# Optimization experiments

Hardware: AMD Instinct MI355X
Metric: run time of the kernel (lower is better)

Reference implementation:

```python
import jax, jax.numpy as jnp
import numpy as np

D_MODEL = 1024
D_STATE = 16
D_CONV = 4
EXPAND = 2
D_INNER = EXPAND * D_MODEL  # 2048
B_SZ = 4
SEQ_L = 2048


def setup_inputs() -> dict:
    key = jax.random.key(0)
    ks = jax.random.split(key, 8)
    x = jax.random.normal(ks[0], (B_SZ, SEQ_L, D_MODEL), dtype=jnp.float32)
    # nn.Linear(d_model, 2*d_inner, bias=False): weight [2*d_inner, d_model]
    W_in = jax.random.normal(ks[1], (2 * D_INNER, D_MODEL), dtype=jnp.float32) * (1.0 / np.sqrt(D_MODEL))
    # depthwise Conv1d weight [d_inner, 1, d_conv] -> stored as [d_inner, d_conv]
    conv_w = jax.random.normal(ks[2], (D_INNER, D_CONV), dtype=jnp.float32) * (1.0 / np.sqrt(D_CONV))
    conv_b = jax.random.normal(ks[3], (D_INNER,), dtype=jnp.float32) * 0.01
    W_out = jax.random.normal(ks[4], (D_MODEL, D_INNER), dtype=jnp.float32) * (1.0 / np.sqrt(D_INNER))
    A = jnp.eye(D_STATE, dtype=jnp.float32)
    Bmat = jax.random.normal(ks[5], (D_STATE, D_INNER), dtype=jnp.float32) * 0.01
    Cmat = jax.random.normal(ks[6], (D_STATE, D_INNER), dtype=jnp.float32) * 0.01
    return {"x": x, "W_in": W_in, "conv_w": conv_w, "conv_b": conv_b,
            "W_out": W_out, "A": A, "Bmat": Bmat, "Cmat": Cmat}


def _causal_depthwise_conv(x_bld, conv_w, conv_b):
    # x_bld: [B, L, C]; conv_w: [C, k]; matches torch Conv1d(groups=C, padding=k-1) sliced to [:L]
    C, k = conv_w.shape
    lhs = jnp.transpose(x_bld, (0, 2, 1))            # [B, C, L]
    rhs = conv_w[:, None, :]                          # [C, 1, k]
    out = jax.lax.conv_general_dilated(
        lhs, rhs, window_strides=(1,), padding=[(k - 1, 0)],
        feature_group_count=C,
        dimension_numbers=("NCH", "OIH", "NCH"))
    out = out + conv_b[None, :, None]
    return jnp.transpose(out, (0, 2, 1))              # [B, L, C]


def reference(x, W_in, conv_w, conv_b, W_out, A, Bmat, Cmat):
    B, L, _ = x.shape
    d_state = A.shape[0]
    xz = x @ W_in.T                                   # [B, L, 2*d_inner]
    x_part, z = jnp.split(xz, 2, axis=-1)             # each [B, L, d_inner]
    x_conv = jax.nn.silu(_causal_depthwise_conv(x_part, conv_w, conv_b))
    # precompute input drive u_t = x_t @ B.T for all t
    u = jnp.einsum("bld,sd->bls", x_part, Bmat)       # [B, L, d_state]

    def step(s, u_t):                                 # s: [B, d_state]
        s = s @ A.T + u_t
        return s, s

    s0 = jnp.zeros((B, d_state), dtype=x.dtype)
    _, states = jax.lax.scan(step, s0, jnp.transpose(u, (1, 0, 2)))  # [L, B, d_state]
    states = jnp.transpose(states, (1, 0, 2))         # [B, L, d_state]
    state_proj = jnp.einsum("bls,sd->bld", states, Cmat)  # [B, L, d_inner]
    y = (x_conv + state_proj) * jax.nn.sigmoid(z)     # [B, L, d_inner]
    return y @ W_out.T                                # [B, L, d_model]
```

## Files before the change

kernel.cpp:

```cpp
#include <hip/hip_runtime.h>

#define D_MODEL 1024
#define D_STATE 16
#define D_CONV  4
#define D_INNER 2048
#define B_SZ    4
#define SEQ_L   2048
#define ROWS    (B_SZ * SEQ_L)
#define N_XZ    (2 * D_INNER)

typedef unsigned short u16;
typedef unsigned int   u32;
typedef float f32x4 __attribute__((ext_vector_type(4)));
typedef short s16x8 __attribute__((ext_vector_type(8)));
typedef u16   u16x8 __attribute__((ext_vector_type(8)));
typedef u16   u16x4 __attribute__((ext_vector_type(4)));

__device__ __forceinline__ u16 f2bf(float f) {
  union { float f; u32 u; } v; v.f = f;
  u32 r = v.u + 0x7fffu + ((v.u >> 16) & 1u);
  return (u16)(r >> 16);
}
__device__ __forceinline__ float bf2f(u16 h) {
  union { u32 u; float f; } v; v.u = ((u32)h) << 16; return v.f;
}
__device__ __forceinline__ float sigmoidf_(float x) {
  return 1.0f / (1.0f + __expf(-x));
}

__global__ __launch_bounds__(256) void k_f2bf4(
    const float* __restrict__ a, u16* __restrict__ ao, int na4,
    const float* __restrict__ b, u16* __restrict__ bo, int nb4,
    const float* __restrict__ c, u16* __restrict__ co, int nc4,
    const float* __restrict__ e, u16* __restrict__ eo, int ne4)
{
  int i = blockIdx.x * 256 + threadIdx.x;
  const float* s; u16* d; int j;
  if (i < na4)                              { s = a; d = ao; j = i; }
  else if (i - na4 < nb4)                   { s = b; d = bo; j = i - na4; }
  else if (i - na4 - nb4 < nc4)             { s = c; d = co; j = i - na4 - nb4; }
  else if (i - na4 - nb4 - nc4 < ne4)       { s = e; d = eo; j = i - na4 - nb4 - nc4; }
  else return;
  f32x4 v = ((const f32x4*)s)[j];
  u16x4 o;
  o[0] = f2bf(v[0]); o[1] = f2bf(v[1]); o[2] = f2bf(v[2]); o[3] = f2bf(v[3]);
  ((u16x4*)d)[j] = o;
}

__global__ __launch_bounds__(512, 2) void k_g201(
    const u16* __restrict__ A,
    const u16* __restrict__ B,
    u16* __restrict__ C,
    int M, int N, int K, int nbx)
{
  __shared__ __align__(16) u16 lA[2][256 * 64];
  __shared__ __align__(16) u16 lB[2][256 * 64];

  const int t    = threadIdx.x;
  const int lane = t & 63;
  const int wave = t >> 6;
  const int wr   = wave >> 2;
  const int wc   = wave & 3;
  const int lrow = lane & 15;
  const int lch  = lane >> 4;

  const int xcd = blockIdx.x & 7;
  const int sub = blockIdx.x >> 3;
  const int msz = (M >> 8) >> 2;
  const int nsz = nbx >> 1;
  const int sm  = sub / nsz;
  const int sn  = sub - sm * nsz;
  const int bm  = ((xcd >> 1) * msz + sm) * 256;
  const int bn  = ((xcd & 1) * nsz + sn) * 256;
  const int NT  = K / 64;

  const int rl0 = t >> 3;
  const int cc  = t & 7;
  int rowG[4][2];
  rowG[0][0] = rl0;        rowG[0][1] = rl0 + 128;
  rowG[1][0] = rl0 + 64;   rowG[1][1] = rl0 + 192;
  rowG[2][0] = rl0;        rowG[2][1] = rl0 + 64;
  rowG[3][0] = rl0 + 128;  rowG[3][1] = rl0 + 192;
  const u16* srcG[4][2];
  u32 dstG[4][2];
#pragma unroll
  for (int g = 0; g < 4; ++g)
#pragma unroll
    for (int i = 0; i < 2; ++i) {
      int row = rowG[g][i];
      const u16* base = (g < 2) ? A + (size_t)(bm + row) * K
                                : B + (size_t)(bn + row) * K;
      srcG[g][i] = base + ((cc ^ (row & 7)) << 3);
      dstG[g][i] = (u32)(row * 64 + cc * 8);
    }

  auto stage = [&](int g, int buf, int kt) {
    u16* dst0 = (g < 2) ? &lA[buf][dstG[g][0]] : &lB[buf][dstG[g][0]];
    u16* dst1 = (g < 2) ? &lA[buf][dstG[g][1]] : &lB[buf][dstG[g][1]];
    __builtin_amdgcn_global_load_lds(
        (const __attribute__((address_space(1))) void*)(srcG[g][0] + kt * 64),
        (__attribute__((address_space(3))) void*)dst0, 16, 0, 0);
    __builtin_amdgcn_global_load_lds(
        (const __attribute__((address_space(1))) void*)(srcG[g][1] + kt * 64),
        (__attribute__((address_space(3))) void*)dst1, 16, 0, 0);
  };

  u32 aoff[8], boff[4], ck[2];
#pragma unroll
  for (int mi = 0; mi < 8; ++mi)
    aoff[mi] = (u32)((wr * 128 + mi * 16 + lrow) * 128);
#pragma unroll
  for (int ni = 0; ni < 4; ++ni)
    boff[ni] = (u32)((wc * 64 + ni * 16 + lrow) * 128);
#pragma unroll
  for (int ks = 0; ks < 2; ++ks)
    ck[ks] = (u32)((((ks * 4 + lch) ^ (lrow & 7)) << 4));
  const u32 baseA = (u32)(size_t)(__attribute__((address_space(3))) void*)&lA[0][0];
  const u32 baseB = (u32)(size_t)(__attribute__((address_space(3))) void*)&lB[0][0];

  f32x4 acc[8][4] = {};
  s16x8 av[4], bv0[4], bv1[4];

  stage(0, 0, 0); stage(1, 0, 0); stage(2, 0, 0); stage(3, 0, 0);
  stage(0, 1, 1); stage(2, 1, 1);
  asm volatile("s_waitcnt vmcnt(4)" ::: "memory");
  __builtin_amdgcn_s_barrier();

  for (int tt = 0; tt < NT; ++tt) {
    const int cur = tt & 1, nxt = cur ^ 1;
    const u32 bA = baseA + (u32)cur * 32768u;
    const u32 bB = baseB + (u32)cur * 32768u;
    const bool s1 = (tt + 1 < NT), s2 = (tt + 2 < NT);

#pragma unroll
    for (int mi = 0; mi < 4; ++mi) {
      u32 ad = bA + aoff[mi] + ck[0];
      asm volatile("ds_read_b128 %0, %1" : "=v"(av[mi]) : "v"(ad));
    }
#pragma unroll
    for (int ni = 0; ni < 4; ++ni) {
      u32 ad = bB + boff[ni] + ck[0];
      asm volatile("ds_read_b128 %0, %1" : "=v"(bv0[ni]) : "v"(ad));
    }
    if (s1) stage(3, nxt, tt + 1);
    __builtin_amdgcn_s_barrier();
    asm volatile("s_waitcnt lgkmcnt(0)" ::: "memory");
    __builtin_amdgcn_sched_barrier(0);
    __builtin_amdgcn_s_setprio(1);
#pragma unroll
    for (int mi = 0; mi < 4; ++mi)
#pragma unroll
      for (int ni = 0; ni < 4; ++ni)
        acc[mi][ni] = __builtin_amdgcn_mfma_f32_16x16x32_bf16(av[mi], bv0[ni], acc[mi][ni], 0, 0, 0);
    __builtin_amdgcn_s_setprio(0);
    __builtin_amdgcn_s_barrier();

#pragma unroll
    for (int mi = 0; mi < 4; ++mi) {
      u32 ad = bA + aoff[mi] + ck[1];
      asm volatile("ds_read_b128 %0, %1" : "=v"(av[mi]) : "v"(ad));
    }
#pragma unroll
    for (int ni = 0; ni < 4; ++ni) {
      u32 ad = bB + boff[ni] + ck[1];
      asm volatile("ds_read_b128 %0, %1" : "=v"(bv1[ni]) : "v"(ad));
    }
    if (s1) stage(1, nxt, tt + 1);
    __builtin_amdgcn_s_barrier();
    asm volatile("s_waitcnt lgkmcnt(0)" ::: "memory");
    __builtin_amdgcn_sched_barrier(0);
    __builtin_amdgcn_s_setprio(1);
#pragma unroll
    for (int mi = 0; mi < 4; ++mi)
#pragma unroll
      for (int ni = 0; ni < 4; ++ni)
        acc[mi][ni] = __builtin_amdgcn_mfma_f32_16x16x32_bf16(av[mi], bv1[ni], acc[mi][ni], 0, 0, 0);
    __builtin_amdgcn_s_setprio(0);
    asm volatile("s_waitcnt vmcnt(6)" ::: "memory");
    __builtin_amdgcn_s_barrier();

#pragma unroll
    for (int mi = 0; mi < 4; ++mi) {
      u32 ad = bA + aoff[4 + mi] + ck[0];
      asm volatile("ds_read_b128 %0, %1" : "=v"(av[mi]) : "v"(ad));
    }
    if (s2) stage(0, cur, tt + 2);
    __builtin_amdgcn_s_barrier();
    asm volatile("s_waitcnt lgkmcnt(0)" ::: "memory");
    __builtin_amdgcn_sched_barrier(0);
    __builtin_amdgcn_s_setprio(1);
#pragma unroll
    for (int mi = 0; mi < 4; ++mi)
#pragma unroll
      for (int ni = 0; ni < 4; ++ni)
        acc[4 + mi][ni] = __builtin_amdgcn_mfma_f32_16x16x32_bf16(av[mi], bv0[ni], acc[4 + mi][ni], 0, 0, 0);
    __builtin_amdgcn_s_setprio(0);
    __builtin_amdgcn_s_barrier();

#pragma unroll
    for (int mi = 0; mi < 4; ++mi) {
      u32 ad = bA + aoff[4 + mi] + ck[1];
      asm volatile("ds_read_b128 %0, %1" : "=v"(av[mi]) : "v"(ad));
    }
    if (s2) stage(2, cur, tt + 2);
    __builtin_amdgcn_s_barrier();
    asm volatile("s_waitcnt lgkmcnt(0)" ::: "memory");
    __builtin_amdgcn_sched_barrier(0);
    __builtin_amdgcn_s_setprio(1);
#pragma unroll
    for (int mi = 0; mi < 4; ++mi)
#pragma unroll
      for (int ni = 0; ni < 4; ++ni)
        acc[4 + mi][ni] = __builtin_amdgcn_mfma_f32_16x16x32_bf16(av[mi], bv1[ni], acc[4 + mi][ni], 0, 0, 0);
    __builtin_amdgcn_s_setprio(0);
    if (s2)      asm volatile("s_waitcnt vmcnt(6)" ::: "memory");
    else if (s1) asm volatile("s_waitcnt vmcnt(0)" ::: "memory");
    __builtin_amdgcn_s_barrier();
  }

  const int crow0 = (lane >> 4) * 4;
#pragma unroll
  for (int mi = 0; mi < 8; ++mi)
#pragma unroll
    for (int ni = 0; ni < 4; ++ni)
#pragma unroll
      for (int r = 0; r < 4; ++r) {
        int row = bm + wr * 128 + mi * 16 + crow0 + r;
        int col = bn + wc * 64 + ni * 16 + lrow;
        C[(size_t)row * N + col] = f2bf(acc[mi][ni][r]);
      }
}

template<bool OUT_BF16>
__global__ __launch_bounds__(256, 2) void k_gemm_f(
    const u16* __restrict__ A, const u16* __restrict__ B,
    void* __restrict__ Cv, int M, int N, int K, int nbx)
{
  __shared__ __align__(16) u16 lA[3][128 * 32];
  __shared__ __align__(16) u16 lB[3][256 * 32];

  const int t    = threadIdx.x;
  const int lane = t & 63;
  const int wave = t >> 6;
  const int wr   = wave >> 1;
  const int wc   = wave & 1;
  const int lrow = lane & 15;
  const int lch  = lane >> 4;

  const int xcd = blockIdx.x & 7;
  const int sub = blockIdx.x >> 3;
  const int msz = (M >> 7) >> 2;
  const int nsz = nbx >> 1;
  const int sm  = sub / nsz;
  const int sn  = sub - sm * nsz;
  const int bm  = ((xcd >> 1) * msz + sm) * 128;
  const int bn  = ((xcd & 1) * nsz + sn) * 256;
  const int NT  = K / 32;

  const int ca0 = t, ca1 = t + 256;
  const u16* srcA0 = A + (size_t)(bm + (ca0 >> 2)) * K + ((ca0 & 3) ^ ((ca0 >> 3) & 3)) * 8;
  const u16* srcA1 = A + (size_t)(bm + (ca1 >> 2)) * K + ((ca1 & 3) ^ ((ca1 >> 3) & 3)) * 8;
  const u16* srcB[4];
#pragma unroll
  for (int i = 0; i < 4; ++i) {
    int c = t + i * 256;
    srcB[i] = B + (size_t)(bn + (c >> 2)) * K + ((c & 3) ^ ((c >> 3) & 3)) * 8;
  }

  auto stageA = [&](int sl, int kt) {
    __builtin_amdgcn_global_load_lds(
        (const __attribute__((address_space(1))) void*)(srcA0 + kt * 32),
        (__attribute__((address_space(3))) void*)&lA[sl][ca0 * 8], 16, 0, 0);
    __builtin_amdgcn_global_load_lds(
        (const __attribute__((address_space(1))) void*)(srcA1 + kt * 32),
        (__attribute__((address_space(3))) void*)&lA[sl][ca1 * 8], 16, 0, 0);
  };
  auto stageB = [&](int sl, int kt) {
#pragma unroll
    for (int i = 0; i < 4; ++i) {
      int c = t + i * 256;
      __builtin_amdgcn_global_load_lds(
          (const __attribute__((address_space(1))) void*)(srcB[i] + kt * 32),
          (__attribute__((address_space(3))) void*)&lB[sl][c * 8], 16, 0, 0);
    }
  };

  u32 offA[4], offB[8];
#pragma unroll
  for (int m = 0; m < 4; ++m) {
    int ra = wr * 64 + m * 16 + lrow;
    offA[m] = (u32)(ra * 64 + ((lch ^ ((ra >> 1) & 3)) << 4));
  }
#pragma unroll
  for (int n = 0; n < 8; ++n) {
    int rb = wc * 128 + n * 16 + lrow;
    offB[n] = (u32)(rb * 64 + ((lch ^ ((rb >> 1) & 3)) << 4));
  }
  const u32 baseA = (u32)(size_t)(__attribute__((address_space(3))) void*)&lA[0][0];
  const u32 baseB = (u32)(size_t)(__attribute__((address_space(3))) void*)&lB[0][0];

  f32x4 acc[4][8] = {};
  s16x8 av[4], bv[8];

  stageA(0, 0); stageB(0, 0);
  stageA(1, 1); stageB(1, 1);
  asm volatile("s_waitcnt vmcnt(6)" ::: "memory");
  __builtin_amdgcn_s_barrier();

  int slot = 0;
  for (int tt = 0; tt < NT; ++tt) {
    const int nslot = (slot == 0) ? 2 : slot - 1;
    const u32 bA = baseA + (u32)slot * 8192u;
    const u32 bB = baseB + (u32)slot * 16384u;
    const bool st = (tt + 2 < NT);
#pragma unroll
    for (int m = 0; m < 4; ++m) {
      u32 ad = bA + offA[m];
      asm volatile("ds_read_b128 %0, %1" : "=v"(av[m]) : "v"(ad));
    }
#pragma unroll
    for (int n = 0; n < 4; ++n) {
      u32 ad = bB + offB[n];
      asm volatile("ds_read_b128 %0, %1" : "=v"(bv[n]) : "v"(ad));
    }
    if (st) stageA(nslot, tt + 2);
    __builtin_amdgcn_s_barrier();
    asm volatile("s_waitcnt lgkmcnt(0)" ::: "memory");
    __builtin_amdgcn_sched_barrier(0);
    __builtin_amdgcn_s_setprio(1);
#pragma unroll
    for (int m = 0; m < 4; ++m)
#pragma unroll
      for (int n = 0; n < 4; ++n)
        acc[m][n] = __builtin_amdgcn_mfma_f32_16x16x32_bf16(av[m], bv[n], acc[m][n], 0, 0, 0);
    __builtin_amdgcn_s_setprio(0);
    __builtin_amdgcn_s_barrier();
#pragma unroll
    for (int n = 4; n < 8; ++n) {
      u32 ad = bB + offB[n];
      asm volatile("ds_read_b128 %0, %1" : "=v"(bv[n]) : "v"(ad));
    }
    if (st) stageB(nslot, tt + 2);
    __builtin_amdgcn_s_barrier();
    asm volatile("s_waitcnt lgkmcnt(0)" ::: "memory");
    __builtin_amdgcn_sched_barrier(0);
    __builtin_amdgcn_s_setprio(1);
#pragma unroll
    for (int m = 0; m < 4; ++m)
#pragma unroll
      for (int n = 4; n < 8; ++n)
        acc[m][n] = __builtin_amdgcn_mfma_f32_16x16x32_bf16(av[m], bv[n], acc[m][n], 0, 0, 0);
    __builtin_amdgcn_s_setprio(0);
    if (st)                asm volatile("s_waitcnt vmcnt(6)" ::: "memory");
    else if (tt + 1 < NT)  asm volatile("s_waitcnt vmcnt(0)" ::: "memory");
    __builtin_amdgcn_s_barrier();
    slot = (slot == 2) ? 0 : slot + 1;
  }

  const int crow0 = (lane >> 4) * 4;
  if constexpr (OUT_BF16) {
    u16* C = (u16*)Cv;
#pragma unroll
    for (int m = 0; m < 4; ++m)
#pragma unroll
      for (int n = 0; n < 8; ++n)
#pragma unroll
        for (int r = 0; r < 4; ++r) {
          int row = bm + wr * 64 + m * 16 + crow0 + r;
          int col = bn + wc * 128 + n * 16 + lrow;
          C[(size_t)row * N + col] = f2bf(acc[m][n][r]);
        }
  } else {
    float* C = (float*)Cv;
#pragma unroll
    for (int m = 0; m < 4; ++m)
#pragma unroll
      for (int n = 0; n < 8; ++n)
#pragma unroll
        for (int r = 0; r < 4; ++r) {
          int row = bm + wr * 64 + m * 16 + crow0 + r;
          int col = bn + wc * 128 + n * 16 + lrow;
          C[(size_t)row * N + col] = acc[m][n][r];
        }
  }
}

__global__ __launch_bounds__(256) void k_u_mfma(
    const u16* __restrict__ xz, const u16* __restrict__ Bbf,
    float* __restrict__ u)
{
  const int lane = threadIdx.x & 63;
  const int wave = threadIdx.x >> 6;
  const int row0 = blockIdx.x * 64 + wave * 16;
  const int ar   = lane & 15;
  const int ak   = (lane >> 4) * 8;
  const u16* xp = xz + (size_t)(row0 + ar) * N_XZ + ak;
  const u16* bp = Bbf + (size_t)ar * D_INNER + ak;
  f32x4 acc = {};
#pragma unroll 8
  for (int k = 0; k < D_INNER; k += 32) {
    s16x8 av = *(const s16x8*)(xp + k);
    s16x8 bv = *(const s16x8*)(bp + k);
    acc = __builtin_amdgcn_mfma_f32_16x16x32_bf16(av, bv, acc, 0, 0, 0);
  }
#pragma unroll
  for (int r = 0; r < 4; ++r)
    u[(size_t)(row0 + (lane >> 4) * 4 + r) * D_STATE + ar] = acc[r];
}

__global__ __launch_bounds__(64) void k_scan(
    const float* __restrict__ u, float* __restrict__ states)
{
  const int blk  = blockIdx.x;
  const int b    = blk >> 4;
  const int s    = blk & 15;
  const int lane = threadIdx.x;
  const float* up = u + (size_t)b * SEQ_L * D_STATE + s;
  float* sp = states + (size_t)b * SEQ_L * D_STATE + s;
  const int t0 = lane * (SEQ_L / 64);
  float v[32];
  float run = 0.0f;
#pragma unroll
  for (int i = 0; i < 32; ++i) { run += up[(size_t)(t0 + i) * D_STATE]; v[i] = run; }
  float tot = run;
  float pre = tot;
#pragma unroll
  for (int off = 1; off < 64; off <<= 1) {
    float n = __shfl_up(pre, off);
    if (lane >= off) pre += n;
  }
  pre -= tot;
#pragma unroll
  for (int i = 0; i < 32; ++i) sp[(size_t)(t0 + i) * D_STATE] = v[i] + pre;
}

__global__ __launch_bounds__(256) void k_fused_y(
    const u16* __restrict__ xz, const float* __restrict__ conv_w,
    const float* __restrict__ conv_b, const float* __restrict__ states,
    const float* __restrict__ Cmat, u16* __restrict__ y)
{
  const int t    = threadIdx.x;
  const int row0 = blockIdx.x * 4;
  const int l0   = row0 & (SEQ_L - 1);
  const int d0   = t * 8;

  float xin[7][8];
#pragma unroll
  for (int r = 0; r < 7; ++r) {
    int l = l0 + r - 3;
    if (l >= 0) {
      u16x8 v = *(const u16x8*)(xz + (size_t)(row0 + r - 3) * N_XZ + d0);
#pragma unroll
      for (int j = 0; j < 8; ++j) xin[r][j] = bf2f(v[j]);
    } else {
#pragma unroll
      for (int j = 0; j < 8; ++j) xin[r][j] = 0.0f;
    }
  }

  float cw[8][4];
#pragma unroll
  for (int j = 0; j < 8; ++j) {
    f32x4 w = ((const f32x4*)conv_w)[d0 + j];
#pragma unroll
    for (int k = 0; k < 4; ++k) cw[j][k] = w[k];
  }
  f32x4 cb0 = *(const f32x4*)(conv_b + d0);
  f32x4 cb1 = *(const f32x4*)(conv_b + d0 + 4);

  float xc[4][8];
#pragma unroll
  for (int rr = 0; rr < 4; ++rr)
#pragma unroll
    for (int j = 0; j < 8; ++j) {
      float v = (j < 4) ? cb0[j] : cb1[j - 4];
#pragma unroll
      for (int k = 0; k < 4; ++k) v += xin[rr + k][j] * cw[j][k];
      xc[rr][j] = v * sigmoidf_(v);
    }

  float st[4][16];
#pragma unroll
  for (int rr = 0; rr < 4; ++rr) {
    const f32x4* s4 = (const f32x4*)(states + (size_t)(row0 + rr) * D_STATE);
#pragma unroll
    for (int q = 0; q < 4; ++q) {
      f32x4 v = s4[q];
      st[rr][q * 4 + 0] = v[0]; st[rr][q * 4 + 1] = v[1];
      st[rr][q * 4 + 2] = v[2]; st[rr][q * 4 + 3] = v[3];
    }
  }
  float sp[4][8] = {};
#pragma unroll
  for (int s = 0; s < 16; ++s) {
    const float* cp = Cmat + (size_t)s * D_INNER + d0;
    f32x4 c0 = *(const f32x4*)cp;
    f32x4 c1 = *(const f32x4*)(cp + 4);
#pragma unroll
    for (int rr = 0; rr < 4; ++rr)
#pragma unroll
      for (int j = 0; j < 4; ++j) {
        sp[rr][j]     += st[rr][s] * c0[j];
        sp[rr][4 + j] += st[rr][s] * c1[j];
      }
  }
#pragma unroll
  for (int rr = 0; rr < 4; ++rr) {
    u16x8 zv = *(const u16x8*)(xz + (size_t)(row0 + rr) * N_XZ + D_INNER + d0);
    u16x8 o;
#pragma unroll
    for (int j = 0; j < 8; ++j)
      o[j] = f2bf((xc[rr][j] + sp[rr][j]) * sigmoidf_(bf2f(zv[j])));
    *(u16x8*)(y + (size_t)(row0 + rr) * D_INNER + d0) = o;
  }
}

extern "C" void kernel_launch(void* const* d_in, const int* in_sizes, int n_in,
                              void* d_out, int out_size, void* d_ws, size_t ws_size,
                              hipStream_t stream) {
  const float* x      = (const float*)d_in[0];
  const float* W_in   = (const float*)d_in[1];
  const float* conv_w = (const float*)d_in[2];
  const float* conv_b = (const float*)d_in[3];
  const float* W_out  = (const float*)d_in[4];
  const float* Bmat   = (const float*)d_in[6];
  const float* Cmat   = (const float*)d_in[7];
  float* out = (float*)d_out;

  char* ws = (char*)d_ws;
  u16*   xzbf   = (u16*)  (ws + 0);
  u16*   ybf    = (u16*)  (ws + 67108864);
  u16*   xbf    = (u16*)  (ws + 100663296);
  u16*   wibf   = (u16*)  (ws + 117440512);
  u16*   wobf   = (u16*)  (ws + 125829120);
  float* u      = (float*)(ws + 130023424);
  float* states = (float*)(ws + 130547712);
  u16*   bmbf   = (u16*)  (ws + 131072000);

  {
    int na4 = ROWS * D_MODEL / 4, nb4 = N_XZ * D_MODEL / 4,
        nc4 = D_MODEL * D_INNER / 4, ne4 = D_STATE * D_INNER / 4;
    int tot = na4 + nb4 + nc4 + ne4;
    k_f2bf4<<<(tot + 255) / 256, 256, 0, stream>>>(
        x, xbf, na4, W_in, wibf, nb4, W_out, wobf, nc4, Bmat, bmbf, ne4);
  }

  k_g201<<<512, 512, 0, stream>>>(xbf, wibf, xzbf, ROWS, N_XZ, D_MODEL, N_XZ / 256);

  k_u_mfma<<<ROWS / 64, 256, 0, stream>>>(xzbf, bmbf, u);
  k_scan<<<B_SZ * D_STATE, 64, 0, stream>>>(u, states);

  k_fused_y<<<ROWS / 4, 256, 0, stream>>>(xzbf, conv_w, conv_b, states, Cmat, ybf);

  k_gemm_f<false><<<256, 256, 0, stream>>>(ybf, wobf, out, ROWS, D_MODEL, D_INNER, D_MODEL / 256);
}
```

Baseline: 191.8 us.

## Fuse x fp32-to-bf16 conversion into input GEMM A-tile staging

```diff
diff --git a/kernel.cpp b/kernel.cpp
--- a/kernel.cpp
+++ b/kernel.cpp
@@ -28,18 +28,16 @@
   return 1.0f / (1.0f + __expf(-x));
 }
 
-__global__ __launch_bounds__(256) void k_f2bf4(
+__global__ __launch_bounds__(256) void k_f2bf3(
     const float* __restrict__ a, u16* __restrict__ ao, int na4,
     const float* __restrict__ b, u16* __restrict__ bo, int nb4,
-    const float* __restrict__ c, u16* __restrict__ co, int nc4,
-    const float* __restrict__ e, u16* __restrict__ eo, int ne4)
+    const float* __restrict__ c, u16* __restrict__ co, int nc4)
 {
   int i = blockIdx.x * 256 + threadIdx.x;
   const float* s; u16* d; int j;
-  if (i < na4)                              { s = a; d = ao; j = i; }
-  else if (i - na4 < nb4)                   { s = b; d = bo; j = i - na4; }
-  else if (i - na4 - nb4 < nc4)             { s = c; d = co; j = i - na4 - nb4; }
-  else if (i - na4 - nb4 - nc4 < ne4)       { s = e; d = eo; j = i - na4 - nb4 - nc4; }
+  if (i < na4)                        { s = a; d = ao; j = i; }
+  else if (i - na4 < nb4)             { s = b; d = bo; j = i - na4; }
+  else if (i - na4 - nb4 < nc4)       { s = c; d = co; j = i - na4 - nb4; }
   else return;
   f32x4 v = ((const f32x4*)s)[j];
   u16x4 o;
@@ -48,7 +46,7 @@
 }
 
 __global__ __launch_bounds__(512, 2) void k_g201(
-    const u16* __restrict__ A,
+    const float* __restrict__ X,
     const u16* __restrict__ B,
     u16* __restrict__ C,
     int M, int N, int K, int nbx)
@@ -74,35 +72,55 @@
   const int bn  = ((xcd & 1) * nsz + sn) * 256;
   const int NT  = K / 64;
 
+  const float* srcA[4];
+  u32 dstA[4];
+#pragma unroll
+  for (int i = 0; i < 4; ++i) {
+    int c    = t + i * 512;
+    int row  = c >> 3;
+    int col8 = c & 7;
+    srcA[i] = X + (size_t)(bm + row) * K + col8 * 8;
+    dstA[i] = (u32)(row * 64 + ((col8 ^ (row & 7)) << 3));
+  }
   const int rl0 = t >> 3;
   const int cc  = t & 7;
-  int rowG[4][2];
-  rowG[0][0] = rl0;        rowG[0][1] = rl0 + 128;
-  rowG[1][0] = rl0 + 64;   rowG[1][1] = rl0 + 192;
-  rowG[2][0] = rl0;        rowG[2][1] = rl0 + 64;
-  rowG[3][0] = rl0 + 128;  rowG[3][1] = rl0 + 192;
-  const u16* srcG[4][2];
-  u32 dstG[4][2];
-#pragma unroll
-  for (int g = 0; g < 4; ++g)
-#pragma unroll
-    for (int i = 0; i < 2; ++i) {
-      int row = rowG[g][i];
-      const u16* base = (g < 2) ? A + (size_t)(bm + row) * K
-                                : B + (size_t)(bn + row) * K;
-      srcG[g][i] = base + ((cc ^ (row & 7)) << 3);
-      dstG[g][i] = (u32)(row * 64 + cc * 8);
-    }
-
-  auto stage = [&](int g, int buf, int kt) {
-    u16* dst0 = (g < 2) ? &lA[buf][dstG[g][0]] : &lB[buf][dstG[g][0]];
-    u16* dst1 = (g < 2) ? &lA[buf][dstG[g][1]] : &lB[buf][dstG[g][1]];
-    __builtin_amdgcn_global_load_lds(
-        (const __attribute__((address_space(1))) void*)(srcG[g][0] + kt * 64),
-        (__attribute__((address_space(3))) void*)dst0, 16, 0, 0);
-    __builtin_amdgcn_global_load_lds(
-        (const __attribute__((address_space(1))) void*)(srcG[g][1] + kt * 64),
-        (__attribute__((address_space(3))) void*)dst1, 16, 0, 0);
+  int rowB[4] = { rl0, rl0 + 64, rl0 + 128, rl0 + 192 };
+  const u16* srcB[4];
+  u32 dstB[4];
+#pragma unroll
+  for (int i = 0; i < 4; ++i) {
+    int row = rowB[i];
+    srcB[i] = B + (size_t)(bn + row) * K + ((cc ^ (row & 7)) << 3);
+    dstB[i] = (u32)(row * 64 + cc * 8);
+  }
+  auto stageB = [&](int buf, int kt) {
+#pragma unroll
+    for (int i = 0; i < 4; ++i)
+      __builtin_amdgcn_global_load_lds(
+          (const __attribute__((address_space(1))) void*)(srcB[i] + kt * 64),
+          (__attribute__((address_space(3))) void*)&lB[buf][dstB[i]], 16, 0, 0);
+  };
+
+  f32x4 ald[4][2];
+  auto loadA = [&](int kt) {
+#pragma unroll
+    for (int i = 0; i < 4; ++i) {
+      const float* p = srcA[i] + kt * 64;
+      ald[i][0] = *(const f32x4*)p;
+      ald[i][1] = *(const f32x4*)(p + 4);
+    }
+  };
+  auto writeA = [&](int buf) {
+#pragma unroll
+    for (int i = 0; i < 4; ++i) {
+      u16x8 w;
+#pragma unroll
+      for (int j = 0; j < 4; ++j) {
+        w[j]     = f2bf(ald[i][0][j]);
+        w[4 + j] = f2bf(ald[i][1][j]);
+      }
+      *(u16x8*)&lA[buf][dstA[i]] = w;
+    }
   };
 
   u32 aoff[8], boff[4], ck[2];
@@ -121,28 +139,44 @@
   f32x4 acc[8][4] = {};
   s16x8 av[4], bv0[4], bv1[4];
 
-  stage(0, 0, 0); stage(1, 0, 0); stage(2, 0, 0); stage(3, 0, 0);
-  stage(0, 1, 1); stage(2, 1, 1);
-  asm volatile("s_waitcnt vmcnt(4)" ::: "memory");
+  loadA(0);
+  stageB(0, 0);
+  f32x4 sav[4][2];
+  {
+#pragma unroll
+    for (int i = 0; i < 4; ++i) {
+      const float* p = srcA[i] + 64;
+      sav[i][0] = *(const f32x4*)p;
+      sav[i][1] = *(const f32x4*)(p + 4);
+    }
+  }
+  stageB(1, 1);
+  asm volatile("s_waitcnt vmcnt(16)" ::: "memory");
+  writeA(0);
+#pragma unroll
+  for (int i = 0; i < 4; ++i) { ald[i][0] = sav[i][0]; ald[i][1] = sav[i][1]; }
+  asm volatile("s_waitcnt vmcnt(8)" ::: "memory");
+  asm volatile("s_waitcnt lgkmcnt(0)" ::: "memory");
+  __builtin_amdgcn_sched_barrier(0);
   __builtin_amdgcn_s_barrier();
 
   for (int tt = 0; tt < NT; ++tt) {
     const int cur = tt & 1, nxt = cur ^ 1;
     const u32 bA = baseA + (u32)cur * 32768u;
     const u32 bB = baseB + (u32)cur * 32768u;
-    const bool s1 = (tt + 1 < NT), s2 = (tt + 2 < NT);
-
+    const bool s1 = (tt + 1 < NT);
+
+#pragma unroll
+    for (int ni = 0; ni < 4; ++ni) {
+      u32 ad = bB + boff[ni] + ck[0];
+      asm volatile("ds_read_b128 %0, %1" : "=v"(bv0[ni]) : "v"(ad));
+    }
 #pragma unroll
     for (int mi = 0; mi < 4; ++mi) {
       u32 ad = bA + aoff[mi] + ck[0];
       asm volatile("ds_read_b128 %0, %1" : "=v"(av[mi]) : "v"(ad));
     }
-#pragma unroll
-    for (int ni = 0; ni < 4; ++ni) {
-      u32 ad = bB + boff[ni] + ck[0];
-      asm volatile("ds_read_b128 %0, %1" : "=v"(bv0[ni]) : "v"(ad));
-    }
-    if (s1) stage(3, nxt, tt + 1);
+    if (s1 && tt > 0) loadA(tt + 1);
     __builtin_amdgcn_s_barrier();
     asm volatile("s_waitcnt lgkmcnt(0)" ::: "memory");
     __builtin_amdgcn_sched_barrier(0);
@@ -156,16 +190,16 @@
     __builtin_amdgcn_s_barrier();
 
 #pragma unroll
+    for (int ni = 0; ni < 4; ++ni) {
+      u32 ad = bB + boff[ni] + ck[1];
+      asm volatile("ds_read_b128 %0, %1" : "=v"(bv1[ni]) : "v"(ad));
+    }
+#pragma unroll
     for (int mi = 0; mi < 4; ++mi) {
       u32 ad = bA + aoff[mi] + ck[1];
       asm volatile("ds_read_b128 %0, %1" : "=v"(av[mi]) : "v"(ad));
     }
-#pragma unroll
-    for (int ni = 0; ni < 4; ++ni) {
-      u32 ad = bB + boff[ni] + ck[1];
-      asm volatile("ds_read_b128 %0, %1" : "=v"(bv1[ni]) : "v"(ad));
-    }
-    if (s1) stage(1, nxt, tt + 1);
+    if (s1 && tt > 0) stageB(nxt, tt + 1);
     __builtin_amdgcn_s_barrier();
     asm volatile("s_waitcnt lgkmcnt(0)" ::: "memory");
     __builtin_amdgcn_sched_barrier(0);
@@ -176,7 +210,6 @@
       for (int ni = 0; ni < 4; ++ni)
         acc[mi][ni] = __builtin_amdgcn_mfma_f32_16x16x32_bf16(av[mi], bv1[ni], acc[mi][ni], 0, 0, 0);
     __builtin_amdgcn_s_setprio(0);
-    asm volatile("s_waitcnt vmcnt(6)" ::: "memory");
     __builtin_amdgcn_s_barrier();
 
 #pragma unroll
@@ -184,7 +217,6 @@
       u32 ad = bA + aoff[4 + mi] + ck[0];
       asm volatile("ds_read_b128 %0, %1" : "=v"(av[mi]) : "v"(ad));
     }
-    if (s2) stage(0, cur, tt + 2);
     __builtin_amdgcn_s_barrier();
     asm volatile("s_waitcnt lgkmcnt(0)" ::: "memory");
     __builtin_amdgcn_sched_barrier(0);
@@ -202,7 +234,11 @@
       u32 ad = bA + aoff[4 + mi] + ck[1];
       asm volatile("ds_read_b128 %0, %1" : "=v"(av[mi]) : "v"(ad));
     }
-    if (s2) stage(2, cur, tt + 2);
+    if (s1) {
+      if (tt > 0) { asm volatile("s_waitcnt vmcnt(4)" ::: "memory"); }
+      else        { asm volatile("s_waitcnt vmcnt(0)" ::: "memory"); }
+      writeA(nxt);
+    }
     __builtin_amdgcn_s_barrier();
     asm volatile("s_waitcnt lgkmcnt(0)" ::: "memory");
     __builtin_amdgcn_sched_barrier(0);
@@ -213,8 +249,7 @@
       for (int ni = 0; ni < 4; ++ni)
         acc[4 + mi][ni] = __builtin_amdgcn_mfma_f32_16x16x32_bf16(av[mi], bv1[ni], acc[4 + mi][ni], 0, 0, 0);
     __builtin_amdgcn_s_setprio(0);
-    if (s2)      asm volatile("s_waitcnt vmcnt(6)" ::: "memory");
-    else if (s1) asm volatile("s_waitcnt vmcnt(0)" ::: "memory");
+    if (s1) asm volatile("s_waitcnt vmcnt(0)" ::: "memory");
     __builtin_amdgcn_s_barrier();
   }
 
@@ -314,14 +349,14 @@
     const u32 bB = baseB + (u32)slot * 16384u;
     const bool st = (tt + 2 < NT);
 #pragma unroll
+    for (int n = 0; n < 4; ++n) {
+      u32 ad = bB + offB[n];
+      asm volatile("ds_read_b128 %0, %1" : "=v"(bv[n]) : "v"(ad));
+    }
+#pragma unroll
     for (int m = 0; m < 4; ++m) {
       u32 ad = bA + offA[m];
       asm volatile("ds_read_b128 %0, %1" : "=v"(av[m]) : "v"(ad));
-    }
-#pragma unroll
-    for (int n = 0; n < 4; ++n) {
-      u32 ad = bB + offB[n];
-      asm volatile("ds_read_b128 %0, %1" : "=v"(bv[n]) : "v"(ad));
     }
     if (st) stageA(nslot, tt + 2);
     __builtin_amdgcn_s_barrier();
@@ -439,24 +474,8 @@
     const float* __restrict__ conv_b, const float* __restrict__ states,
     const float* __restrict__ Cmat, u16* __restrict__ y)
 {
-  const int t    = threadIdx.x;
-  const int row0 = blockIdx.x * 4;
-  const int l0   = row0 & (SEQ_L - 1);
-  const int d0   = t * 8;
-
-  float xin[7][8];
-#pragma unroll
-  for (int r = 0; r < 7; ++r) {
-    int l = l0 + r - 3;
-    if (l >= 0) {
-      u16x8 v = *(const u16x8*)(xz + (size_t)(row0 + r - 3) * N_XZ + d0);
-#pragma unroll
-      for (int j = 0; j < 8; ++j) xin[r][j] = bf2f(v[j]);
-    } else {
-#pragma unroll
-      for (int j = 0; j < 8; ++j) xin[r][j] = 0.0f;
-    }
-  }
+  const int t  = threadIdx.x;
+  const int d0 = t * 8;
 
   float cw[8][4];
 #pragma unroll
@@ -468,50 +487,69 @@
   f32x4 cb0 = *(const f32x4*)(conv_b + d0);
   f32x4 cb1 = *(const f32x4*)(conv_b + d0 + 4);
 
-  float xc[4][8];
-#pragma unroll
-  for (int rr = 0; rr < 4; ++rr)
-#pragma unroll
-    for (int j = 0; j < 8; ++j) {
-      float v = (j < 4) ? cb0[j] : cb1[j - 4];
-#pragma unroll
-      for (int k = 0; k < 4; ++k) v += xin[rr + k][j] * cw[j][k];
-      xc[rr][j] = v * sigmoidf_(v);
-    }
-
-  float st[4][16];
-#pragma unroll
-  for (int rr = 0; rr < 4; ++rr) {
-    const f32x4* s4 = (const f32x4*)(states + (size_t)(row0 + rr) * D_STATE);
-#pragma unroll
-    for (int q = 0; q < 4; ++q) {
-      f32x4 v = s4[q];
-      st[rr][q * 4 + 0] = v[0]; st[rr][q * 4 + 1] = v[1];
-      st[rr][q * 4 + 2] = v[2]; st[rr][q * 4 + 3] = v[3];
-    }
-  }
-  float sp[4][8] = {};
-#pragma unroll
-  for (int s = 0; s < 16; ++s) {
-    const float* cp = Cmat + (size_t)s * D_INNER + d0;
-    f32x4 c0 = *(const f32x4*)cp;
-    f32x4 c1 = *(const f32x4*)(cp + 4);
+  for (int ch = 0; ch < 4; ++ch) {
+    const int row0 = blockIdx.x * 16 + ch * 4;
+    const int l0   = row0 & (SEQ_L - 1);
+
+    float xin[7][8];
+#pragma unroll
+    for (int r = 0; r < 7; ++r) {
+      int l = l0 + r - 3;
+      if (l >= 0) {
+        u16x8 v = *(const u16x8*)(xz + (size_t)(row0 + r - 3) * N_XZ + d0);
+#pragma unroll
+        for (int j = 0; j < 8; ++j) xin[r][j] = bf2f(v[j]);
+      } else {
+#pragma unroll
+        for (int j = 0; j < 8; ++j) xin[r][j] = 0.0f;
+      }
+    }
+
+    float xc[4][8];
 #pragma unroll
     for (int rr = 0; rr < 4; ++rr)
 #pragma unroll
-      for (int j = 0; j < 4; ++j) {
-        sp[rr][j]     += st[rr][s] * c0[j];
-        sp[rr][4 + j] += st[rr][s] * c1[j];
+      for (int j = 0; j < 8; ++j) {
+        float v = (j < 4) ? cb0[j] : cb1[j - 4];
+#pragma unroll
+        for (int k = 0; k < 4; ++k) v += xin[rr + k][j] * cw[j][k];
+        xc[rr][j] = v * sigmoidf_(v);
       }
-  }
-#pragma unroll
-  for (int rr = 0; rr < 4; ++rr) {
-    u16x8 zv = *(const u16x8*)(xz + (size_t)(row0 + rr) * N_XZ + D_INNER + d0);
-    u16x8 o;
-#pragma unroll
-    for (int j = 0; j < 8; ++j)
-      o[j] = f2bf((xc[rr][j] + sp[rr][j]) * sigmoidf_(bf2f(zv[j])));
-    *(u16x8*)(y + (size_t)(row0 + rr) * D_INNER + d0) = o;
+
+    float st[4][16];
+#pragma unroll
+    for (int rr = 0; rr < 4; ++rr) {
+      const f32x4* s4 = (const f32x4*)(states + (size_t)(row0 + rr) * D_STATE);
+#pragma unroll
+      for (int q = 0; q < 4; ++q) {
+        f32x4 v = s4[q];
+        st[rr][q * 4 + 0] = v[0]; st[rr][q * 4 + 1] = v[1];
+        st[rr][q * 4 + 2] = v[2]; st[rr][q * 4 + 3] = v[3];
+      }
+    }
+    float sp[4][8] = {};
+#pragma unroll
+    for (int s = 0; s < 16; ++s) {
+      const float* cp = Cmat + (size_t)s * D_INNER + d0;
+      f32x4 c0 = *(const f32x4*)cp;
+      f32x4 c1 = *(const f32x4*)(cp + 4);
+#pragma unroll
+      for (int rr = 0; rr < 4; ++rr)
+#pragma unroll
+        for (int j = 0; j < 4; ++j) {
+          sp[rr][j]     += st[rr][s] * c0[j];
+          sp[rr][4 + j] += st[rr][s] * c1[j];
+        }
+    }
+#pragma unroll
+    for (int rr = 0; rr < 4; ++rr) {
+      u16x8 zv = *(const u16x8*)(xz + (size_t)(row0 + rr) * N_XZ + D_INNER + d0);
+      u16x8 o;
+#pragma unroll
+      for (int j = 0; j < 8; ++j)
+        o[j] = f2bf((xc[rr][j] + sp[rr][j]) * sigmoidf_(bf2f(zv[j])));
+      *(u16x8*)(y + (size_t)(row0 + rr) * D_INNER + d0) = o;
+    }
   }
 }
 
@@ -530,7 +568,6 @@
   char* ws = (char*)d_ws;
   u16*   xzbf   = (u16*)  (ws + 0);
   u16*   ybf    = (u16*)  (ws + 67108864);
-  u16*   xbf    = (u16*)  (ws + 100663296);
   u16*   wibf   = (u16*)  (ws + 117440512);
   u16*   wobf   = (u16*)  (ws + 125829120);
   float* u      = (float*)(ws + 130023424);
@@ -538,19 +575,19 @@
   u16*   bmbf   = (u16*)  (ws + 131072000);
 
   {
-    int na4 = ROWS * D_MODEL / 4, nb4 = N_XZ * D_MODEL / 4,
-        nc4 = D_MODEL * D_INNER / 4, ne4 = D_STATE * D_INNER / 4;
-    int tot = na4 + nb4 + nc4 + ne4;
-    k_f2bf4<<<(tot + 255) / 256, 256, 0, stream>>>(
-        x, xbf, na4, W_in, wibf, nb4, W_out, wobf, nc4, Bmat, bmbf, ne4);
-  }
-
-  k_g201<<<512, 512, 0, stream>>>(xbf, wibf, xzbf, ROWS, N_XZ, D_MODEL, N_XZ / 256);
+    int na4 = N_XZ * D_MODEL / 4, nb4 = D_MODEL * D_INNER / 4,
+        nc4 = D_STATE * D_INNER / 4;
+    int tot = na4 + nb4 + nc4;
+    k_f2bf3<<<(tot + 255) / 256, 256, 0, stream>>>(
+        W_in, wibf, na4, W_out, wobf, nb4, Bmat, bmbf, nc4);
+  }
+
+  k_g201<<<512, 512, 0, stream>>>(x, wibf, xzbf, ROWS, N_XZ, D_MODEL, N_XZ / 256);
 
   k_u_mfma<<<ROWS / 64, 256, 0, stream>>>(xzbf, bmbf, u);
   k_scan<<<B_SZ * D_STATE, 64, 0, stream>>>(u, states);
 
-  k_fused_y<<<ROWS / 4, 256, 0, stream>>>(xzbf, conv_w, conv_b, states, Cmat, ybf);
+  k_fused_y<<<ROWS / 16, 256, 0, stream>>>(xzbf, conv_w, conv_b, states, Cmat, ybf);
 
   k_gemm_f<false><<<256, 256, 0, stream>>>(ybf, wobf, out, ROWS, D_MODEL, D_INNER, D_MODEL / 256);
 }
```

After: 198.6 us. 1.04x slower.
